# Performance work log

Measured on AMD Instinct MI355X. Metric: run time of the kernel, lower is better.

Reference implementation:

```python
import jax, jax.numpy as jnp
import numpy as np

N, IN_DIM, OUT_DIM = 8192, 128, 64
ALPHA = 0.2  # LeakyReLU negative slope
NEG_INF = -1e12


def setup_inputs() -> dict:
    key = jax.random.key(0)
    k1, k2, k3, k4 = jax.random.split(key, 4)
    x = jax.random.normal(k1, (N, IN_DIM), dtype=jnp.float32)
    adj = jax.random.randint(k2, (N, N), 0, 2, dtype=jnp.int32)
    W = jax.random.normal(k3, (IN_DIM, OUT_DIM), dtype=jnp.float32) * 0.1
    a = jax.random.normal(k4, (2 * OUT_DIM, 1), dtype=jnp.float32) * 0.1
    return {"x": x, "adj": adj, "W": W, "a": a}


def reference(x, adj, W, a):
    Wh = x @ W                                   # [N, out_dim]
    Wh1 = Wh @ a[:OUT_DIM, :]                    # [N, 1] source scores
    Wh2 = Wh @ a[OUT_DIM:, :]                    # [N, 1] target scores
    e = Wh1 + Wh2.T                              # [N, N] additive attention
    e = jnp.where(e > 0, e, ALPHA * e)           # LeakyReLU
    scores = jnp.where(adj > 0, e, NEG_INF)      # mask non-edges
    attention = jax.nn.softmax(scores, axis=1)   # row-wise softmax
    h_prime = attention @ Wh                     # [N, out_dim]
    return jax.nn.elu(h_prime)
```

## Files before the change

kernel.cpp:

```cpp
#include <hip/hip_runtime.h>


#define N 8192
#define IN_DIM 128
#define OUT_DIM 64
#define ALPHA 0.2f
#define LOG2E 1.44269504088896f
#define JC 8
#define CW (N / JC)
#define TW 128
#define NT (CW / TW)
#define LDP 136

typedef _Float16 half8 __attribute__((ext_vector_type(8)));
typedef _Float16 half4 __attribute__((ext_vector_type(4)));
typedef float f32x4 __attribute__((ext_vector_type(4)));

__global__ __launch_bounds__(64) void wh_kernel(
    const float* __restrict__ x, const float* __restrict__ W,
    const float* __restrict__ a, _Float16* __restrict__ Wh_t,
    float* __restrict__ s1L, float* __restrict__ s2L) {
  __shared__ float xs[IN_DIM];
  const int i = blockIdx.x;
  const int t = threadIdx.x;

  xs[t]      = x[(size_t)i * IN_DIM + t];
  xs[t + 64] = x[(size_t)i * IN_DIM + 64 + t];
  __syncthreads();

  float wh = 0.f;
#pragma unroll
  for (int d = 0; d < IN_DIM; ++d) wh = fmaf(xs[d], W[d * OUT_DIM + t], wh);

  Wh_t[(size_t)t * N + i] = (_Float16)wh;

  float p1 = wh * a[t];
  float p2 = wh * a[64 + t];
#pragma unroll
  for (int off = 32; off; off >>= 1) {
    p1 += __shfl_down(p1, off);
    p2 += __shfl_down(p2, off);
  }
  if (t == 0) {
    s1L[i] = p1 * LOG2E;
    s2L[i] = p2 * LOG2E;
  }
}

__global__ __launch_bounds__(256) void max_kernel(
    const float* __restrict__ s1L, const float* __restrict__ s2L,
    float* __restrict__ c0out) {
  __shared__ float red[8];
  const int t = threadIdx.x;
  float m1 = -1e30f, m2 = -1e30f;
  for (int idx = t; idx < N; idx += 256) {
    m1 = fmaxf(m1, s1L[idx]);
    m2 = fmaxf(m2, s2L[idx]);
  }
#pragma unroll
  for (int off = 32; off; off >>= 1) {
    m1 = fmaxf(m1, __shfl_down(m1, off));
    m2 = fmaxf(m2, __shfl_down(m2, off));
  }
  if ((t & 63) == 0) {
    red[t >> 6] = m1;
    red[4 + (t >> 6)] = m2;
  }
  __syncthreads();
  if (t == 0) {
    m1 = fmaxf(fmaxf(red[0], red[1]), fmaxf(red[2], red[3]));
    m2 = fmaxf(fmaxf(red[4], red[5]), fmaxf(red[6], red[7]));
    float e = m1 + m2;
    c0out[0] = exp2f(-fmaxf(e, ALPHA * e));
  }
}

__global__ __launch_bounds__(256) void bpack_kernel(
    const _Float16* __restrict__ Wh_t, _Float16* __restrict__ Bpack) {
  const int kt = blockIdx.x;
  const int t = threadIdx.x;
  const int fg = t >> 6;
  const int lane = t & 63;
  const int q = (t >> 4) & 3;
  const int r16 = t & 15;
  const half8 v =
      *(const half8*)(Wh_t + (size_t)(fg * 16 + r16) * N + kt * 32 + q * 8);
  *(half8*)(Bpack + ((size_t)(kt * 4 + fg) * 64 + lane) * 8) = v;
}

__global__ __launch_bounds__(256, 4) void attn_kernel(
    const int* __restrict__ adj, const _Float16* __restrict__ Bpack,
    const float* __restrict__ s1L, const float* __restrict__ s2L,
    const float* __restrict__ c0p, float* __restrict__ accp,
    float* __restrict__ lp) {
  __shared__ __align__(16) _Float16 Ps[4 * 16 * LDP];

  const int t = threadIdx.x;
  const int w = t >> 6;
  const int lane = t & 63;
  const int q = lane >> 4;
  const int r16 = lane & 15;
  const int half_ = lane >> 5;
  const int l32 = lane & 31;
  const int rb = (int)(gridDim.x - 1 - blockIdx.x);
  const int i0 = rb * 64 + w * 16;
  const int c = blockIdx.y;
  const int jb = c * CW;

  const float c0 = c0p[0];

  float s1v8[8];
#pragma unroll
  for (int it = 0; it < 8; ++it) s1v8[it] = s1L[i0 + 2 * it + half_];

  half8 bones;
#pragma unroll
  for (int e = 0; e < 8; ++e)
    bones[e] = (r16 == 0) ? (_Float16)1.0f : (_Float16)0.0f;

  f32x4 acc[5] = {{0.f, 0.f, 0.f, 0.f}, {0.f, 0.f, 0.f, 0.f},
                  {0.f, 0.f, 0.f, 0.f}, {0.f, 0.f, 0.f, 0.f},
                  {0.f, 0.f, 0.f, 0.f}};

  const int* aprow = adj + (size_t)(i0 + half_) * N + jb + l32 * 4;
  _Float16* Pw = Ps + w * 16 * LDP;
  const _Float16* ldA = Pw + r16 * LDP + q * 8;
  _Float16* stP = Pw + half_ * LDP + l32 * 4;

  int4 av[8];
#pragma unroll
  for (int it = 0; it < 8; ++it)
    av[it] = *(const int4*)(aprow + (size_t)(2 * it) * N);

  for (int jt = 0; jt < NT; ++jt) {
    const int j0 = jb + jt * TW;
    const int joff_next = ((jt + 1) & (NT - 1)) * TW;

    int4 nv[8];
#pragma unroll
    for (int it = 0; it < 8; ++it)
      nv[it] = *(const int4*)(aprow + joff_next + (size_t)(2 * it) * N);

    const float4 sv = *(const float4*)(s2L + j0 + l32 * 4);

#pragma unroll
    for (int it = 0; it < 8; ++it) {
      const float s1v = s1v8[it];
      float tt, uu;
      half4 hv;
      tt = s1v + sv.x; uu = fmaxf(tt, ALPHA * tt);
      hv[0] = (_Float16)(av[it].x != 0 ? exp2f(uu) * c0 : 0.f);
      tt = s1v + sv.y; uu = fmaxf(tt, ALPHA * tt);
      hv[1] = (_Float16)(av[it].y != 0 ? exp2f(uu) * c0 : 0.f);
      tt = s1v + sv.z; uu = fmaxf(tt, ALPHA * tt);
      hv[2] = (_Float16)(av[it].z != 0 ? exp2f(uu) * c0 : 0.f);
      tt = s1v + sv.w; uu = fmaxf(tt, ALPHA * tt);
      hv[3] = (_Float16)(av[it].w != 0 ? exp2f(uu) * c0 : 0.f);
      *(half4*)(stP + (2 * it) * LDP) = hv;
    }

    const int ktb = c * 32 + jt * 4;
#pragma unroll
    for (int ks = 0; ks < 4; ++ks) {
      const half8 aF = *(const half8*)(ldA + ks * 32);
      const _Float16* bp = Bpack + ((size_t)(ktb + ks) * 4 * 64 + lane) * 8;
#pragma unroll
      for (int fg = 0; fg < 4; ++fg) {
        const half8 bf = *(const half8*)(bp + (size_t)fg * 64 * 8);
        acc[fg] =
            __builtin_amdgcn_mfma_f32_16x16x32_f16(aF, bf, acc[fg], 0, 0, 0);
      }
      acc[4] =
          __builtin_amdgcn_mfma_f32_16x16x32_f16(aF, bones, acc[4], 0, 0, 0);
    }

#pragma unroll
    for (int it = 0; it < 8; ++it) av[it] = nv[it];
  }

#pragma unroll
  for (int fg = 0; fg < 4; ++fg) {
#pragma unroll
    for (int r = 0; r < 4; ++r) {
      accp[((size_t)c * N + i0 + q * 4 + r) * OUT_DIM + fg * 16 + r16] =
          acc[fg][r];
    }
  }
  if (r16 == 0) {
#pragma unroll
    for (int r = 0; r < 4; ++r) lp[(size_t)c * N + i0 + q * 4 + r] = acc[4][r];
  }
}

__global__ __launch_bounds__(256) void reduce_kernel(
    const float* __restrict__ accp, const float* __restrict__ lp,
    float* __restrict__ out) {
  const int tid = blockIdx.x * 256 + threadIdx.x;
  const int i = tid >> 6;
  float s = 0.f, l = 0.f;
#pragma unroll
  for (int c = 0; c < JC; ++c) s += accp[(size_t)c * N * OUT_DIM + tid];
#pragma unroll
  for (int c = 0; c < JC; ++c) l += lp[(size_t)c * N + i];
  float v = s / l;
  out[tid] = v > 0.f ? v : expm1f(v);
}

extern "C" void kernel_launch(void* const* d_in, const int* in_sizes, int n_in,
                              void* d_out, int out_size, void* d_ws,
                              size_t ws_size, hipStream_t stream) {
  const float* x = (const float*)d_in[0];
  const int* adj = (const int*)d_in[1];
  const float* W = (const float*)d_in[2];
  const float* a = (const float*)d_in[3];
  float* out = (float*)d_out;

  char* ws = (char*)d_ws;
  _Float16* Wh_t = (_Float16*)ws;
  float* s1L = (float*)(ws + (1u << 20));
  float* s2L = s1L + N;
  float* c0 = s2L + N;
  _Float16* Bpack = (_Float16*)(ws + (2u << 20));
  float* accp = (float*)(ws + (4u << 20));
  float* lp = accp + (size_t)JC * N * OUT_DIM;

  wh_kernel<<<N, 64, 0, stream>>>(x, W, a, Wh_t, s1L, s2L);
  max_kernel<<<1, 256, 0, stream>>>(s1L, s2L, c0);
  bpack_kernel<<<N / 32, 256, 0, stream>>>(Wh_t, Bpack);
  attn_kernel<<<dim3(N / 64, JC), 256, 0, stream>>>(adj, Bpack, s1L, s2L, c0,
                                                    accp, lp);
  reduce_kernel<<<N * OUT_DIM / 256, 256, 0, stream>>>(accp, lp, out);
}
```

Measured before the change: 407.0 us.

## Factor exp of LeakyReLU into precomputed fp16 row/column tables with packed math

Rewrites exp2(leaky(s1+s2)) as max(f1[i]*t1[j], f2[i]*t2[j]) using per-node exponent tables built in a new ftab kernel. The inner loop then uses packed fp16 multiplies and max, plus a bitmask multiply for adjacency, instead of per-element exp2. It also halves the tile width, doubles the column split JC, and hoists the B-fragment loads ahead of the elementwise work. fp16 products of the separated factors can overflow or underflow where the fused exponent would not, which risks accuracy. The larger JC also doubles the partial-sum traffic in the reduce step.

```diff
diff --git a/kernel.cpp b/kernel.cpp
--- a/kernel.cpp
+++ b/kernel.cpp
@@ -6,14 +6,14 @@
 #define OUT_DIM 64
 #define ALPHA 0.2f
 #define LOG2E 1.44269504088896f
-#define JC 8
+#define JC 16
 #define CW (N / JC)
-#define TW 128
+#define TW 64
 #define NT (CW / TW)
-#define LDP 136
+#define LDP 72
 
 typedef _Float16 half8 __attribute__((ext_vector_type(8)));
-typedef _Float16 half4 __attribute__((ext_vector_type(4)));
+typedef _Float16 h2 __attribute__((ext_vector_type(2)));
 typedef float f32x4 __attribute__((ext_vector_type(4)));
 
 __global__ __launch_bounds__(64) void wh_kernel(
@@ -49,7 +49,7 @@
 
 __global__ __launch_bounds__(256) void max_kernel(
     const float* __restrict__ s1L, const float* __restrict__ s2L,
-    float* __restrict__ c0out) {
+    float* __restrict__ mm) {
   __shared__ float red[8];
   const int t = threadIdx.x;
   float m1 = -1e30f, m2 = -1e30f;
@@ -71,8 +71,27 @@
     m1 = fmaxf(fmaxf(red[0], red[1]), fmaxf(red[2], red[3]));
     m2 = fmaxf(fmaxf(red[4], red[5]), fmaxf(red[6], red[7]));
     float e = m1 + m2;
-    c0out[0] = exp2f(-fmaxf(e, ALPHA * e));
-  }
+    mm[0] = m1;
+    mm[1] = fmaxf(e, ALPHA * e);
+  }
+}
+
+__global__ __launch_bounds__(256) void ftab_kernel(
+    const float* __restrict__ s1L, const float* __restrict__ s2L,
+    const float* __restrict__ mm, unsigned int* __restrict__ Fi,
+    _Float16* __restrict__ TTh) {
+  const int j = blockIdx.x * 256 + threadIdx.x;
+  const float m1 = mm[0], ML = mm[1];
+
+  const _Float16 f1 = (_Float16)exp2f(s1L[j] - m1);
+  const _Float16 f2 = (_Float16)exp2f(0.2f * (s1L[j] - m1));
+  h2 f;
+  f[0] = f1;
+  f[1] = f2;
+  Fi[j] = __builtin_bit_cast(unsigned int, f);
+
+  TTh[(j >> 2) * 8 + (j & 3)]     = (_Float16)exp2f(s2L[j] - (ML - m1));
+  TTh[(j >> 2) * 8 + 4 + (j & 3)] = (_Float16)exp2f(0.2f * s2L[j] - (ML - 0.2f * m1));
 }
 
 __global__ __launch_bounds__(256) void bpack_kernel(
@@ -90,9 +109,8 @@
 
 __global__ __launch_bounds__(256, 4) void attn_kernel(
     const int* __restrict__ adj, const _Float16* __restrict__ Bpack,
-    const float* __restrict__ s1L, const float* __restrict__ s2L,
-    const float* __restrict__ c0p, float* __restrict__ accp,
-    float* __restrict__ lp) {
+    const unsigned int* __restrict__ Fi, const uint4* __restrict__ TT,
+    float* __restrict__ accp, float* __restrict__ lp) {
   __shared__ __align__(16) _Float16 Ps[4 * 16 * LDP];
 
   const int t = threadIdx.x;
@@ -100,18 +118,20 @@
   const int lane = t & 63;
   const int q = lane >> 4;
   const int r16 = lane & 15;
-  const int half_ = lane >> 5;
-  const int l32 = lane & 31;
+  const int r4 = lane >> 4;
+  const int l16 = lane & 15;
   const int rb = (int)(gridDim.x - 1 - blockIdx.x);
   const int i0 = rb * 64 + w * 16;
   const int c = blockIdx.y;
   const int jb = c * CW;
 
-  const float c0 = c0p[0];
-
-  float s1v8[8];
-#pragma unroll
-  for (int it = 0; it < 8; ++it) s1v8[it] = s1L[i0 + 2 * it + half_];
+  h2 f1b[4], f2b[4];
+#pragma unroll
+  for (int it = 0; it < 4; ++it) {
+    const unsigned int u = Fi[i0 + 4 * it + r4];
+    f1b[it] = __builtin_bit_cast(h2, (u & 0xFFFFu) * 0x00010001u);
+    f2b[it] = __builtin_bit_cast(h2, (u >> 16) * 0x00010001u);
+  }
 
   half8 bones;
 #pragma unroll
@@ -122,60 +142,69 @@
                   {0.f, 0.f, 0.f, 0.f}, {0.f, 0.f, 0.f, 0.f},
                   {0.f, 0.f, 0.f, 0.f}};
 
-  const int* aprow = adj + (size_t)(i0 + half_) * N + jb + l32 * 4;
+  const int* ap = adj + (size_t)(i0 + r4) * N + jb + l16 * 4;
   _Float16* Pw = Ps + w * 16 * LDP;
   const _Float16* ldA = Pw + r16 * LDP + q * 8;
-  _Float16* stP = Pw + half_ * LDP + l32 * 4;
-
-  int4 av[8];
-#pragma unroll
-  for (int it = 0; it < 8; ++it)
-    av[it] = *(const int4*)(aprow + (size_t)(2 * it) * N);
+  _Float16* stP = Pw + r4 * LDP + l16 * 4;
+
+  int4 av[4];
+#pragma unroll
+  for (int it = 0; it < 4; ++it) av[it] = *(const int4*)(ap + it * 4 * N);
+  uint4 tt = TT[(jb >> 2) + l16];
 
   for (int jt = 0; jt < NT; ++jt) {
-    const int j0 = jb + jt * TW;
-    const int joff_next = ((jt + 1) & (NT - 1)) * TW;
-
-    int4 nv[8];
-#pragma unroll
-    for (int it = 0; it < 8; ++it)
-      nv[it] = *(const int4*)(aprow + joff_next + (size_t)(2 * it) * N);
-
-    const float4 sv = *(const float4*)(s2L + j0 + l32 * 4);
-
-#pragma unroll
-    for (int it = 0; it < 8; ++it) {
-      const float s1v = s1v8[it];
-      float tt, uu;
-      half4 hv;
-      tt = s1v + sv.x; uu = fmaxf(tt, ALPHA * tt);
-      hv[0] = (_Float16)(av[it].x != 0 ? exp2f(uu) * c0 : 0.f);
-      tt = s1v + sv.y; uu = fmaxf(tt, ALPHA * tt);
-      hv[1] = (_Float16)(av[it].y != 0 ? exp2f(uu) * c0 : 0.f);
-      tt = s1v + sv.z; uu = fmaxf(tt, ALPHA * tt);
-      hv[2] = (_Float16)(av[it].z != 0 ? exp2f(uu) * c0 : 0.f);
-      tt = s1v + sv.w; uu = fmaxf(tt, ALPHA * tt);
-      hv[3] = (_Float16)(av[it].w != 0 ? exp2f(uu) * c0 : 0.f);
-      *(half4*)(stP + (2 * it) * LDP) = hv;
+    const int ktb = c * 16 + jt * 2;
+
+    half8 bf[2][4];
+#pragma unroll
+    for (int ks = 0; ks < 2; ++ks)
+#pragma unroll
+      for (int fg = 0; fg < 4; ++fg)
+        bf[ks][fg] = *(const half8*)(Bpack +
+                                     ((size_t)((ktb + ks) * 4 + fg) * 64 + lane) * 8);
+
+    const int jnoff = ((jt + 1) & (NT - 1)) * TW;
+    int4 nav[4];
+#pragma unroll
+    for (int it = 0; it < 4; ++it)
+      nav[it] = *(const int4*)(ap + jnoff + it * 4 * N);
+    const uint4 ntt = TT[((jb + jnoff) >> 2) + l16];
+
+#pragma unroll
+    for (int it = 0; it < 4; ++it) {
+      const unsigned int mlo =
+          (unsigned int)(av[it].x | (av[it].y << 16)) * 0x3C00u;
+      const unsigned int mhi =
+          (unsigned int)(av[it].z | (av[it].w << 16)) * 0x3C00u;
+      const h2 t1lo = __builtin_bit_cast(h2, tt.x);
+      const h2 t1hi = __builtin_bit_cast(h2, tt.y);
+      const h2 t2lo = __builtin_bit_cast(h2, tt.z);
+      const h2 t2hi = __builtin_bit_cast(h2, tt.w);
+      h2 plo = __builtin_elementwise_max(f1b[it] * t1lo, f2b[it] * t2lo) *
+               __builtin_bit_cast(h2, mlo);
+      h2 phi = __builtin_elementwise_max(f1b[it] * t1hi, f2b[it] * t2hi) *
+               __builtin_bit_cast(h2, mhi);
+      uint2 pw;
+      pw.x = __builtin_bit_cast(unsigned int, plo);
+      pw.y = __builtin_bit_cast(unsigned int, phi);
+      *(uint2*)(stP + it * 4 * LDP) = pw;
     }
 
-    const int ktb = c * 32 + jt * 4;
-#pragma unroll
-    for (int ks = 0; ks < 4; ++ks) {
+#pragma unroll
+    for (int ks = 0; ks < 2; ++ks) {
       const half8 aF = *(const half8*)(ldA + ks * 32);
-      const _Float16* bp = Bpack + ((size_t)(ktb + ks) * 4 * 64 + lane) * 8;
-#pragma unroll
-      for (int fg = 0; fg < 4; ++fg) {
-        const half8 bf = *(const half8*)(bp + (size_t)fg * 64 * 8);
+#pragma unroll
+      for (int fg = 0; fg < 4; ++fg)
         acc[fg] =
-            __builtin_amdgcn_mfma_f32_16x16x32_f16(aF, bf, acc[fg], 0, 0, 0);
-      }
+            __builtin_amdgcn_mfma_f32_16x16x32_f16(aF, bf[ks][fg], acc[fg],
+                                                   0, 0, 0);
       acc[4] =
           __builtin_amdgcn_mfma_f32_16x16x32_f16(aF, bones, acc[4], 0, 0, 0);
     }
 
 #pragma unroll
-    for (int it = 0; it < 8; ++it) av[it] = nv[it];
+    for (int it = 0; it < 4; ++it) av[it] = nav[it];
+    tt = ntt;
   }
 
 #pragma unroll
@@ -219,15 +248,18 @@
   _Float16* Wh_t = (_Float16*)ws;
   float* s1L = (float*)(ws + (1u << 20));
   float* s2L = s1L + N;
-  float* c0 = s2L + N;
+  float* mm = s2L + N;
   _Float16* Bpack = (_Float16*)(ws + (2u << 20));
+  unsigned int* Fi = (unsigned int*)(ws + (3u << 20));
+  _Float16* TTh = (_Float16*)(ws + (3u << 20) + (512u << 10));
   float* accp = (float*)(ws + (4u << 20));
   float* lp = accp + (size_t)JC * N * OUT_DIM;
 
   wh_kernel<<<N, 64, 0, stream>>>(x, W, a, Wh_t, s1L, s2L);
-  max_kernel<<<1, 256, 0, stream>>>(s1L, s2L, c0);
+  max_kernel<<<1, 256, 0, stream>>>(s1L, s2L, mm);
+  ftab_kernel<<<N / 256, 256, 0, stream>>>(s1L, s2L, mm, Fi, TTh);
   bpack_kernel<<<N / 32, 256, 0, stream>>>(Wh_t, Bpack);
-  attn_kernel<<<dim3(N / 64, JC), 256, 0, stream>>>(adj, Bpack, s1L, s2L, c0,
-                                                    accp, lp);
+  attn_kernel<<<dim3(N / 64, JC), 256, 0, stream>>>(
+      adj, Bpack, Fi, (const uint4*)TTh, accp, lp);
   reduce_kernel<<<N * OUT_DIM / 256, 256, 0, stream>>>(accp, lp, out);
 }
```

New measurement: 429.1 us. +5.4%, slower.
